# Kernel tuning notes

Hardware: AMD Instinct MI355X
Metric: run time of the kernel (lower is better)

Reference implementation:

```python
import jax, jax.numpy as jnp
import numpy as np

B, N, DIM = 16, 1024, 768


def setup_inputs() -> dict:
    key = jax.random.key(0)
    ks = jax.random.split(key, 8)
    x = jax.random.normal(ks[0], (B, N, DIM), dtype=jnp.float32)
    y = jax.random.normal(ks[1], (B, N, DIM), dtype=jnp.float32)
    coords = jax.random.normal(ks[2], (N, N, 6), dtype=jnp.float32)
    # orthogonal init for U (as in torch init.orthogonal_)
    a = jax.random.normal(ks[3], (DIM, DIM), dtype=jnp.float32)
    q, r = jnp.linalg.qr(a)
    U = q * jnp.sign(jnp.diagonal(r))[None, :]
    S1 = jnp.ones((DIM,), dtype=jnp.float32)
    S2 = jnp.ones((DIM,), dtype=jnp.float32)
    gating = jnp.asarray(1.0, dtype=jnp.float32)
    temp = jnp.asarray(0.1, dtype=jnp.float32)
    pos_emb = jnp.zeros((N, 6, 1), dtype=jnp.float32)
    return {"x": x, "y": y, "coords": coords, "U": U, "S1": S1, "S2": S2,
            "gating": gating, "temp": temp, "pos_emb": pos_emb}


def reference(x, y, coords, U, S1, S2, gating, temp, pos_emb):
    dim = x.shape[-1]
    scale = dim ** (-0.5)
    # spectral decomposition: x @ U^T @ diag(S^2) @ U
    xu = x @ U.T                                   # [B,N,d]
    x1 = (xu * jnp.square(S1)) @ U                 # [B,N,d]
    x2 = (xu * jnp.square(S2)) @ U                 # [B,N,d]
    xs = jnp.stack([x1, x2], axis=1)               # [B,2,N,d]
    patch_score = jax.nn.softmax(
        jnp.einsum('bknd,bmd->bknm', xs, y) * scale, axis=-1)  # [B,2,N,M]
    pos = jnp.squeeze(coords @ pos_emb, -1)        # [N,M]
    pos_score = jax.nn.softmax(pos, axis=-1)[None, None]        # [1,1,N,M]
    g = jax.nn.sigmoid(gating)
    attn = (1.0 - g) * patch_score + g * pos_score  # [B,2,N,M]
    # entropy-routed gating
    entropy = jnp.sum(-attn * jnp.log(attn + 1e-8), axis=-1)    # [B,2,N]
    hmap = 2.0 - 2.0 * jax.nn.sigmoid(temp * jnp.transpose(entropy, (0, 2, 1)))  # [B,N,2]
    fgbg = hmap[..., 0] >= hmap[..., 1]
    route = jax.lax.stop_gradient(
        jnp.stack([fgbg, ~fgbg], axis=-1).astype(hmap.dtype))   # [B,N,2]
    heat_map = jnp.sum(hmap * route, axis=-1, keepdims=True)    # [B,N,1]
    attn_c = jnp.sum(attn * jnp.transpose(route, (0, 2, 1))[..., None], axis=1)  # [B,N,M]
    out = attn_c @ y                               # [B,N,d]
    return (out, heat_map)
```

## Files before the change

### kernel.cpp

```cpp
#include <hip/hip_runtime.h>
#include <hip/hip_bf16.h>

#define DEV __device__ __forceinline__

typedef unsigned short u16;
typedef short short8 __attribute__((ext_vector_type(8)));
typedef float f32x16 __attribute__((ext_vector_type(16)));

static const int BB = 16;
static const int NN = 1024;
static const int DD = 768;

DEV u16 f2bf(float f) {
    unsigned u = __builtin_bit_cast(unsigned, f);
    unsigned r = u + 0x7fffu + ((u >> 16) & 1u);
    return (u16)(r >> 16);
}
DEV float h2f(u16 u) { return (float)__builtin_bit_cast(_Float16, u); }
DEV u16 f2h(float f) { return __builtin_bit_cast(u16, (_Float16)f); }

DEV short8 ldf8_bf(const float* p) {
    float4 f0 = *(const float4*)p;
    float4 f1 = *(const float4*)(p + 4);
    short8 r;
    r[0] = (short)f2bf(f0.x); r[1] = (short)f2bf(f0.y);
    r[2] = (short)f2bf(f0.z); r[3] = (short)f2bf(f0.w);
    r[4] = (short)f2bf(f1.x); r[5] = (short)f2bf(f1.y);
    r[6] = (short)f2bf(f1.z); r[7] = (short)f2bf(f1.w);
    return r;
}

DEV void gl_lds16(const void* g, void* l) {
    __builtin_amdgcn_global_load_lds(
        (const __attribute__((address_space(1))) unsigned int*)g,
        (__attribute__((address_space(3))) unsigned int*)l, 16, 0, 0);
}

DEV unsigned pkbf_rtz(float f0, float f1) {
    return __builtin_amdgcn_perm(__builtin_bit_cast(unsigned, f1),
                                 __builtin_bit_cast(unsigned, f0), 0x07060302u);
}

DEV void fence_bar() {
    asm volatile("" ::: "memory");
    __builtin_amdgcn_s_barrier();
    asm volatile("" ::: "memory");
}
DEV void wait_vm4() { asm volatile("s_waitcnt vmcnt(4)" ::: "memory"); }

template<int OM>
__global__ __launch_bounds__(256, 3) void gemm128(
    const u16* __restrict__ Ag, const u16* __restrict__ Bg, void* __restrict__ Cg,
    int K, int N, int zmod,
    long sA0, long sA1, long sB0, long sB1, long sC0, long sC1,
    float scale)
{
    __shared__ u16 As[128 * 64];
    __shared__ u16 Bs[128 * 64];

    int z = blockIdx.z;
    const u16* A = Ag + (long)(z % zmod) * sA0 + (long)(z / zmod) * sA1;
    const u16* B = Bg + (long)(z % zmod) * sB0 + (long)(z / zmod) * sB1;
    u16*   Cu = (u16*)Cg   + (long)(z % zmod) * sC0 + (long)(z / zmod) * sC1;
    float* Cf = (float*)Cg + (long)(z % zmod) * sC0 + (long)(z / zmod) * sC1;

    int tid  = threadIdx.x;
    int lane = tid & 63, wave = tid >> 6;
    int wm = wave & 1, wn = wave >> 1;
    int ln31 = lane & 31, khalf = lane >> 5;

    long m0 = (long)blockIdx.x * 128;
    long n0 = (long)blockIdx.y * 128;

    long aOfs[4], bOfs[4];
    u16 *lA[4], *lB[4];
#pragma unroll
    for (int i = 0; i < 4; i++) {
        int p = tid + i * 256;
        int row = p >> 3, qs = p & 7;
        int q = qs ^ (row & 7);
        aOfs[i] = (m0 + row) * (long)K + q * 8;
        bOfs[i] = (n0 + row) * (long)K + q * 8;
        lA[i] = As + p * 8;
        lB[i] = Bs + p * 8;
    }

    int aoff[2][4], boff[2][4];
#pragma unroll
    for (int t = 0; t < 2; t++) {
        int ra = wm * 64 + t * 32 + ln31;
        int rb = wn * 64 + t * 32 + ln31;
#pragma unroll
        for (int h = 0; h < 4; h++) {
            aoff[t][h] = ra * 64 + (((h * 2 + khalf) ^ (ra & 7)) * 8);
            boff[t][h] = rb * 64 + (((h * 2 + khalf) ^ (rb & 7)) * 8);
        }
    }

    f32x16 acc[2][2] = {};

    for (int k0 = 0; k0 < K; k0 += 64) {
#pragma unroll
        for (int i = 0; i < 4; i++) gl_lds16(A + aOfs[i] + k0, lA[i]);
#pragma unroll
        for (int i = 0; i < 4; i++) gl_lds16(B + bOfs[i] + k0, lB[i]);
        __syncthreads();

#pragma unroll
        for (int h = 0; h < 4; h++) {
            short8 af[2], bfr[2];
#pragma unroll
            for (int t = 0; t < 2; t++) af[t]  = *(const short8*)(As + aoff[t][h]);
#pragma unroll
            for (int t = 0; t < 2; t++) bfr[t] = *(const short8*)(Bs + boff[t][h]);
#pragma unroll
            for (int ti = 0; ti < 2; ti++)
#pragma unroll
                for (int tj = 0; tj < 2; tj++)
                    acc[ti][tj] = __builtin_amdgcn_mfma_f32_32x32x16_bf16(
                        af[ti], bfr[tj], acc[ti][tj], 0, 0, 0);
        }
        __syncthreads();
    }

    long crow = m0 + wm * 64 + 4 * khalf;
    long ccol = n0 + wn * 64 + ln31;
#pragma unroll
    for (int ti = 0; ti < 2; ti++)
#pragma unroll
        for (int tj = 0; tj < 2; tj++)
#pragma unroll
            for (int r = 0; r < 16; r++) {
                long row = crow + ti * 32 + (r & 3) + 8 * (r >> 2);
                long col = ccol + tj * 32;
                float v = acc[ti][tj][r] * scale;
                long idx = row * (long)N + col;
                if constexpr (OM == 0)      Cu[idx] = f2bf(v);
                else if constexpr (OM == 1) Cu[idx] = f2h(v);
                else                        Cf[idx] = v;
            }
}

template<int OM>
__global__ __launch_bounds__(512, 2) void gemm256(
    const u16* __restrict__ Ag, const u16* __restrict__ Bg, void* __restrict__ Cg,
    int K, int N, int zmod,
    long sA0, long sA1, long sB0, long sB1, long sC0, long sC1,
    float scale)
{
    __shared__ u16 lds[2][4][8192];

    int z = blockIdx.z;
    const u16* A = Ag + (long)(z % zmod) * sA0 + (long)(z / zmod) * sA1;
    const u16* B = Bg + (long)(z % zmod) * sB0 + (long)(z / zmod) * sB1;
    u16*   Cu = (u16*)Cg   + (long)(z % zmod) * sC0 + (long)(z / zmod) * sC1;
    float* Cf = (float*)Cg + (long)(z % zmod) * sC0 + (long)(z / zmod) * sC1;

    int tid  = threadIdx.x;
    int lane = tid & 63, wave = tid >> 6;
    int wm = wave >> 2, wn = wave & 3;
    int ln31 = lane & 31, khalf = lane >> 5;

    long m0 = (long)blockIdx.x * 256;
    long n0 = (long)blockIdx.y * 256;
    const u16* Apan = A + m0 * (long)K;
    const u16* Bpan = B + n0 * (long)K;

    long stA[2];
#pragma unroll
    for (int r = 0; r < 2; r++) {
        int p = tid + r * 512;
        int row = p >> 2, c = (p & 3) ^ ((row >> 1) & 3);
        stA[r] = (long)row * K + c * 8;
    }

    int aoffs[4][2], boffs[2][2];
#pragma unroll
    for (int m = 0; m < 4; m++) {
        int rr = wm * 128 + m * 32 + ln31;
#pragma unroll
        for (int sl = 0; sl < 2; sl++)
            aoffs[m][sl] = rr * 32 + (((sl * 2 + khalf) ^ ((rr >> 1) & 3)) * 8);
    }
#pragma unroll
    for (int n = 0; n < 2; n++) {
        int cc = wn * 64 + n * 32 + ln31;
#pragma unroll
        for (int sl = 0; sl < 2; sl++)
            boffs[n][sl] = cc * 32 + (((sl * 2 + khalf) ^ ((cc >> 1) & 3)) * 8);
    }

    f32x16 acc[4][2] = {};

    int nkt = K >> 6;
    int niter = nkt >> 1;

#define STG(PAN, BUF, HSEL, KT, KH) do {                                   \
    const u16* _s0 = (PAN) + stA[0] + (long)(KT) * 64 + (KH) * 32;         \
    const u16* _s1 = (PAN) + stA[1] + (long)(KT) * 64 + (KH) * 32;         \
    u16* _d = &lds[BUF][HSEL][0] + tid * 8;                                \
    gl_lds16(_s0, _d);                                                     \
    gl_lds16(_s1, _d + 4096);                                              \
} while (0)

#define PH(BUF, S, DOSTG, GUARD) do {                                      \
    short8 av[4], bv[2];                                                   \
    _Pragma("unroll")                                                      \
    for (int m = 0; m < 4; m++)                                            \
        av[m] = *(const short8*)(&lds[BUF][(S) >> 1][aoffs[m][(S) & 1]]);  \
    _Pragma("unroll")                                                      \
    for (int n = 0; n < 2; n++)                                            \
        bv[n] = *(const short8*)(&lds[BUF][2 + ((S) >> 1)][boffs[n][(S) & 1]]); \
    DOSTG;                                                                 \
    if (GUARD) wait_vm4();                                                 \
    fence_bar();                                                           \
    __builtin_amdgcn_s_setprio(1);                                         \
    _Pragma("unroll")                                                      \
    for (int m = 0; m < 4; m++)                                            \
        _Pragma("unroll")                                                  \
        for (int n = 0; n < 2; n++)                                        \
            acc[m][n] = __builtin_amdgcn_mfma_f32_32x32x16_bf16(           \
                av[m], bv[n], acc[m][n], 0, 0, 0);                         \
    __builtin_amdgcn_s_setprio(0);                                         \
    fence_bar();                                                           \
} while (0)

    STG(Apan, 0, 0, 0, 0);
    STG(Bpan, 0, 2, 0, 0);
    STG(Apan, 0, 1, 0, 1);
    STG(Bpan, 0, 3, 0, 1);
    STG(Apan, 1, 0, 1, 0);
    STG(Bpan, 1, 2, 1, 0);
    wait_vm4();
    fence_bar();

    for (int it = 0; it < niter; ++it) {
        int t1 = 2 * it + 1;
        int t2 = 2 * it + 2; int t2c = t2 < nkt ? t2 : nkt - 1;
        int t3 = 2 * it + 3; int t3c = t3 < nkt ? t3 : nkt - 1;
        PH(0, 0, STG(Apan, 1, 1, t1,  1), false);
        PH(0, 1, STG(Bpan, 1, 3, t1,  1), false);
        PH(0, 2, STG(Apan, 0, 0, t2c, 0), false);
        PH(0, 3, STG(Bpan, 0, 2, t2c, 0), true);
        PH(1, 0, STG(Apan, 0, 1, t2c, 1), false);
        PH(1, 1, STG(Bpan, 0, 3, t2c, 1), false);
        PH(1, 2, STG(Apan, 1, 0, t3c, 0), false);
        PH(1, 3, STG(Bpan, 1, 2, t3c, 0), true);
    }
#undef PH
#undef STG

    long crow = m0 + wm * 128 + 4 * khalf;
    long ccol = n0 + wn * 64 + ln31;
#pragma unroll
    for (int m = 0; m < 4; m++)
#pragma unroll
        for (int n = 0; n < 2; n++)
#pragma unroll
            for (int r = 0; r < 16; r++) {
                long row = crow + m * 32 + (r & 3) + 8 * (r >> 2);
                long col = ccol + n * 32;
                float v = acc[m][n][r] * scale;
                long idx = row * (long)N + col;
                if constexpr (OM == 0)      Cu[idx] = f2bf(v);
                else if constexpr (OM == 1) Cu[idx] = f2h(v);
                else                        Cf[idx] = v;
            }
}

__global__ __launch_bounds__(256, 3) void gemm_f32a(
    const float* __restrict__ Ag, const u16* __restrict__ Bg, u16* __restrict__ Cg,
    int K, int N, long sB0, long sC0)
{
    __shared__ float As[128 * 64];
    __shared__ u16   Bs[128 * 64];

    int z = blockIdx.z;
    const u16* B = Bg + (long)z * sB0;
    u16* Cu = Cg + (long)z * sC0;

    int tid  = threadIdx.x;
    int lane = tid & 63, wave = tid >> 6;
    int wm = wave & 1, wn = wave >> 1;
    int ln31 = lane & 31, khalf = lane >> 5;

    long m0 = (long)blockIdx.x * 128;
    long n0 = (long)blockIdx.y * 128;

    long aOfs[8]; float* lA[8];
#pragma unroll
    for (int i = 0; i < 8; i++) {
        int p = tid + i * 256;
        int row = p >> 4, q = (p & 15) ^ (row & 15);
        aOfs[i] = (m0 + row) * (long)K + q * 4;
        lA[i] = As + p * 4;
    }
    long bOfs[4]; u16* lB[4];
#pragma unroll
    for (int i = 0; i < 4; i++) {
        int p = tid + i * 256;
        int row = p >> 3, q = (p & 7) ^ (row & 7);
        bOfs[i] = (n0 + row) * (long)K + q * 8;
        lB[i] = Bs + p * 8;
    }

    int aoff[2][4][2], boff[2][4];
#pragma unroll
    for (int t = 0; t < 2; t++) {
        int ra = wm * 64 + t * 32 + ln31;
        int rb = wn * 64 + t * 32 + ln31;
#pragma unroll
        for (int h = 0; h < 4; h++) {
            int c0 = h * 4 + khalf * 2;
            aoff[t][h][0] = ra * 64 + ((c0 ^ (ra & 15)) * 4);
            aoff[t][h][1] = ra * 64 + (((c0 + 1) ^ (ra & 15)) * 4);
            boff[t][h] = rb * 64 + (((h * 2 + khalf) ^ (rb & 7)) * 8);
        }
    }

    f32x16 acc[2][2] = {};

    for (int k0 = 0; k0 < K; k0 += 64) {
#pragma unroll
        for (int i = 0; i < 8; i++) gl_lds16(Ag + aOfs[i] + k0, lA[i]);
#pragma unroll
        for (int i = 0; i < 4; i++) gl_lds16(B + bOfs[i] + k0, lB[i]);
        __syncthreads();

#pragma unroll
        for (int h = 0; h < 4; h++) {
            short8 af[2], bfr[2];
#pragma unroll
            for (int t = 0; t < 2; t++) {
                float4 v0 = *(const float4*)(As + aoff[t][h][0]);
                float4 v1 = *(const float4*)(As + aoff[t][h][1]);
                uint4 wv;
                wv.x = pkbf_rtz(v0.x, v0.y);
                wv.y = pkbf_rtz(v0.z, v0.w);
                wv.z = pkbf_rtz(v1.x, v1.y);
                wv.w = pkbf_rtz(v1.z, v1.w);
                af[t] = __builtin_bit_cast(short8, wv);
            }
#pragma unroll
            for (int t = 0; t < 2; t++) bfr[t] = *(const short8*)(Bs + boff[t][h]);
#pragma unroll
            for (int ti = 0; ti < 2; ti++)
#pragma unroll
                for (int tj = 0; tj < 2; tj++)
                    acc[ti][tj] = __builtin_amdgcn_mfma_f32_32x32x16_bf16(
                        af[ti], bfr[tj], acc[ti][tj], 0, 0, 0);
        }
        __syncthreads();
    }

    long crow = m0 + wm * 64 + 4 * khalf;
    long ccol = n0 + wn * 64 + ln31;
#pragma unroll
    for (int ti = 0; ti < 2; ti++)
#pragma unroll
        for (int tj = 0; tj < 2; tj++)
#pragma unroll
            for (int r = 0; r < 16; r++) {
                long row = crow + ti * 32 + (r & 3) + 8 * (r >> 2);
                long col = ccol + tj * 32;
                Cu[row * (long)N + col] = f2bf(acc[ti][tj][r]);
            }
}

DEV float wave_red_max(float v) {
#pragma unroll
    for (int o = 32; o; o >>= 1) v = fmaxf(v, __shfl_xor(v, o));
    return v;
}
DEV float wave_red_sum(float v) {
#pragma unroll
    for (int o = 32; o; o >>= 1) v += __shfl_xor(v, o);
    return v;
}
DEV float block_red_max(float v, float* sh) {
    v = wave_red_max(v);
    if ((threadIdx.x & 63) == 0) sh[threadIdx.x >> 6] = v;
    __syncthreads();
    v = fmaxf(fmaxf(sh[0], sh[1]), fmaxf(sh[2], sh[3]));
    __syncthreads();
    return v;
}
DEV float block_red_sum(float v, float* sh) {
    v = wave_red_sum(v);
    if ((threadIdx.x & 63) == 0) sh[threadIdx.x >> 6] = v;
    __syncthreads();
    v = (sh[0] + sh[1]) + (sh[2] + sh[3]);
    __syncthreads();
    return v;
}
DEV float red2_max(float v, float* sh) {
    v = wave_red_max(v);
    if ((threadIdx.x & 63) == 0) sh[threadIdx.x >> 6] = v;
    __syncthreads();
    v = fmaxf(sh[0], sh[1]);
    __syncthreads();
    return v;
}
DEV float red2_sum(float v, float* sh) {
    v = wave_red_sum(v);
    if ((threadIdx.x & 63) == 0) sh[threadIdx.x >> 6] = v;
    __syncthreads();
    v = sh[0] + sh[1];
    __syncthreads();
    return v;
}

__global__ __launch_bounds__(256) void k_prep_all(
    const float* __restrict__ y,
    const float* __restrict__ coords, const float* __restrict__ U,
    const float* __restrict__ S1, const float* __restrict__ S2,
    const float* __restrict__ pe,
    u16* __restrict__ yb, u16* __restrict__ yT,
    u16* __restrict__ UTb, u16* __restrict__ VT1, u16* __restrict__ VT2,
    float* __restrict__ P)
{
    __shared__ float shmem[32 * 33];
    int bid = blockIdx.x, tid = threadIdx.x;

    if (bid < 12288) {
        float (*tile)[33] = (float(*)[33])shmem;
        int b = bid / 768, rem = bid % 768;
        int d0 = (rem % 24) * 32, m0 = (rem / 24) * 32;
        int tx = tid & 31, ty = tid >> 5;
        const float* ybase = y + (long)b * NN * DD;
#pragma unroll
        for (int r = 0; r < 32; r += 8) {
            int m = m0 + ty + r, d = d0 + tx;
            float v = ybase[(long)m * DD + d];
            tile[ty + r][tx] = v;
            yb[(long)b * NN * DD + (long)m * DD + d] = f2bf(v);
        }
        __syncthreads();
#pragma unroll
        for (int r = 0; r < 32; r += 8) {
            int d = d0 + ty + r, m = m0 + tx;
            yT[(long)b * DD * NN + (long)d * NN + m] = f2bf(tile[tx][ty + r]);
        }
        return;
    }
    bid -= 12288;

    if (bid < 1024) {
        int n = bid, t = tid;
        float p6[6];
#pragma unroll
        for (int c = 0; c < 6; c++) p6[c] = pe[n * 6 + c];
        float v[4];
#pragma unroll
        for (int i = 0; i < 4; i++) {
            const float* cp = coords + ((long)n * NN + t * 4 + i) * 6;
            v[i] = p6[0]*cp[0] + p6[1]*cp[1] + p6[2]*cp[2]
                 + p6[3]*cp[3] + p6[4]*cp[4] + p6[5]*cp[5];
        }
        float mx = block_red_max(fmaxf(fmaxf(v[0], v[1]), fmaxf(v[2], v[3])), shmem);
        float e[4], s = 0.f;
#pragma unroll
        for (int i = 0; i < 4; i++) { e[i] = expf(v[i] - mx); s += e[i]; }
        float Z = block_red_sum(s, shmem);
        float inv = 1.f / Z;
        float4 o; o.x = e[0]*inv; o.y = e[1]*inv; o.z = e[2]*inv; o.w = e[3]*inv;
        *(float4*)(P + ((long)n << 10) + t * 4) = o;
        return;
    }
    bid -= 1024;

    {
        float (*tile)[33] = (float(*)[33])shmem;
        int i0 = (bid % 24) * 32, j0 = (bid / 24) * 32;
        int tx = tid & 31, ty = tid >> 5;
#pragma unroll
        for (int r = 0; r < 32; r += 8) {
            int i = i0 + ty + r, j = j0 + tx;
            tile[ty + r][tx] = U[(long)i * DD + j];
        }
        __syncthreads();
        float s1v = S1[i0 + tx];
        float s2v = S2[i0 + tx];
        s1v *= s1v; s2v *= s2v;
#pragma unroll
        for (int r = 0; r < 32; r += 8) {
            int j = j0 + ty + r, i = i0 + tx;
            float v = tile[tx][ty + r];
            UTb[(long)j * DD + i] = f2bf(v);
            VT1[(long)j * DD + i] = f2bf(s1v * v);
            VT2[(long)j * DD + i] = f2bf(s2v * v);
        }
    }
}

__global__ __launch_bounds__(128) void k_route(
    u16* __restrict__ S, const float* __restrict__ P,
    const float* __restrict__ gating, const float* __restrict__ temp,
    float* __restrict__ heat)
{
    __shared__ float sh[2];
    int bn = blockIdx.x;
    int b = bn >> 10, n = bn & 1023, t = threadIdx.x;
    u16* s1p = S + ((long)(b * 2) << 20) + ((long)n << 10) + t * 8;
    u16* s2p = s1p + (1L << 20);
    const float* pp = P + ((long)n << 10) + t * 8;

    short8 r1 = *(const short8*)s1p;
    short8 r2 = *(const short8*)s2p;
    float4 pv0 = *(const float4*)pp;
    float4 pv1 = *(const float4*)(pp + 4);
    float s1[8], s2[8], p8[8];
#pragma unroll
    for (int i = 0; i < 8; i++) {
        s1[i] = h2f((u16)r1[i]);
        s2[i] = h2f((u16)r2[i]);
    }
    p8[0]=pv0.x; p8[1]=pv0.y; p8[2]=pv0.z; p8[3]=pv0.w;
    p8[4]=pv1.x; p8[5]=pv1.y; p8[6]=pv1.z; p8[7]=pv1.w;

    float m1 = s1[0], m2 = s2[0];
#pragma unroll
    for (int i = 1; i < 8; i++) { m1 = fmaxf(m1, s1[i]); m2 = fmaxf(m2, s2[i]); }
    float mx1 = red2_max(m1, sh);
    float mx2 = red2_max(m2, sh);

    float e1[8], e2[8], z1 = 0.f, z2 = 0.f;
#pragma unroll
    for (int i = 0; i < 8; i++) {
        e1[i] = expf(s1[i] - mx1); z1 += e1[i];
        e2[i] = expf(s2[i] - mx2); z2 += e2[i];
    }
    float Z1 = red2_sum(z1, sh);
    float Z2 = red2_sum(z2, sh);

    float g = 1.f / (1.f + expf(-gating[0]));
    float c1 = (1.f - g) / Z1, c2 = (1.f - g) / Z2;

    float a1[8], a2[8], hh1 = 0.f, hh2 = 0.f;
#pragma unroll
    for (int i = 0; i < 8; i++) {
        a1[i] = e1[i] * c1 + g * p8[i];
        a2[i] = e2[i] * c2 + g * p8[i];
        hh1 -= a1[i] * logf(a1[i] + 1e-8f);
        hh2 -= a2[i] * logf(a2[i] + 1e-8f);
    }
    float H1 = red2_sum(hh1, sh);
    float H2 = red2_sum(hh2, sh);

    float tv = temp[0];
    float hm0 = 2.f - 2.f / (1.f + expf(-tv * H1));
    float hm1 = 2.f - 2.f / (1.f + expf(-tv * H2));
    int ks = (hm0 >= hm1) ? 0 : 1;
    if (t == 0) heat[bn] = ks ? hm1 : hm0;

    short8 w;
#pragma unroll
    for (int i = 0; i < 8; i++) w[i] = (short)f2bf(ks ? a2[i] : a1[i]);
    *(short8*)s1p = w;
}

extern "C" void kernel_launch(void* const* d_in, const int* in_sizes, int n_in,
                              void* d_out, int out_size, void* d_ws, size_t ws_size,
                              hipStream_t stream)
{
    (void)in_sizes; (void)n_in; (void)out_size; (void)ws_size;
    const float* x      = (const float*)d_in[0];
    const float* y      = (const float*)d_in[1];
    const float* coords = (const float*)d_in[2];
    const float* U      = (const float*)d_in[3];
    const float* S1     = (const float*)d_in[4];
    const float* S2     = (const float*)d_in[5];
    const float* gating = (const float*)d_in[6];
    const float* temp   = (const float*)d_in[7];
    const float* pose   = (const float*)d_in[8];

    float* out  = (float*)d_out;
    float* heat = out + (long)BB * NN * DD;

    char* w = (char*)d_ws;
    u16* UTb = (u16*)w;  w += (long)DD * DD * 2;
    u16* VT  = (u16*)w;  w += (long)2 * DD * DD * 2;
    u16* W2  = (u16*)w;  w += (long)2 * DD * DD * 2;
    u16* x12 = (u16*)w;  w += (long)2 * BB * NN * DD * 2;
    u16* yb  = (u16*)w;  w += (long)BB * NN * DD * 2;
    u16* yT  = (u16*)w;  w += (long)BB * DD * NN * 2;
    u16* S   = (u16*)w;  w += (long)BB * 2 * NN * NN * 2;
    float* P = (float*)w;

    const long MBN = (long)BB * NN * DD;
    const long BND = (long)NN * DD;
    const long SPL = (long)NN * NN;
    const long DSQ = (long)DD * DD;

    k_prep_all<<<dim3(13888), dim3(256), 0, stream>>>(
        y, coords, U, S1, S2, pose, yb, yT, UTb, VT, VT + DSQ, P);

    gemm128<0><<<dim3(DD / 128, DD / 128, 2), dim3(256), 0, stream>>>(
        UTb, VT, W2, DD, DD, 2,
        0L, 0L, DSQ, 0L, DSQ, 0L, 1.0f);

    gemm_f32a<<<dim3(BB * NN / 128, DD / 128, 2), dim3(256), 0, stream>>>(
        x, W2, x12, DD, DD, DSQ, MBN);

    gemm256<1><<<dim3(NN / 256, NN / 256, BB * 2), dim3(512), 0, stream>>>(
        x12, yb, S, DD, NN, 2,
        MBN, BND, 0L, BND, SPL, 2 * SPL, 0.036084391824351615f);

    k_route<<<dim3(BB * NN), dim3(128), 0, stream>>>(S, P, gating, temp, heat);

    gemm256<2><<<dim3(NN / 256, DD / 256, BB), dim3(512), 0, stream>>>(
        S, yT, out, NN, DD, 1,
        0L, 2 * SPL, 0L, BND, 0L, BND, 1.0f);
}
```

Before: 371.1 us.

## Pre-convert x to bf16 and use gemm256 for projection; single-wave routing

Adds an x-to-bf16 conversion stage inside the prep kernel, writing into the S workspace that is not yet in use. The x@W2 projection then runs through the larger bf16 gemm256 kernel in place of the fp32-A gemm128 variant that converted inside LDS. The y transpose/convert path is vectorised to float4 and u16x4 accesses. The routing kernel is shrunk to one 64-thread wave per row, with shuffle-only reductions in place of LDS-plus-barrier ones. The trade-off is an extra pass over x (fp32 read, bf16 write) and a change from truncating to round-to-nearest bf16 conversion of x.

```diff
diff --git a/kernel.cpp b/kernel.cpp
--- a/kernel.cpp
+++ b/kernel.cpp
@@ -5,6 +5,7 @@
 
 typedef unsigned short u16;
 typedef short short8 __attribute__((ext_vector_type(8)));
+typedef u16 u16x4 __attribute__((ext_vector_type(4)));
 typedef float f32x16 __attribute__((ext_vector_type(16)));
 
 static const int BB = 16;
@@ -19,26 +20,10 @@
 DEV float h2f(u16 u) { return (float)__builtin_bit_cast(_Float16, u); }
 DEV u16 f2h(float f) { return __builtin_bit_cast(u16, (_Float16)f); }
 
-DEV short8 ldf8_bf(const float* p) {
-    float4 f0 = *(const float4*)p;
-    float4 f1 = *(const float4*)(p + 4);
-    short8 r;
-    r[0] = (short)f2bf(f0.x); r[1] = (short)f2bf(f0.y);
-    r[2] = (short)f2bf(f0.z); r[3] = (short)f2bf(f0.w);
-    r[4] = (short)f2bf(f1.x); r[5] = (short)f2bf(f1.y);
-    r[6] = (short)f2bf(f1.z); r[7] = (short)f2bf(f1.w);
-    return r;
-}
-
 DEV void gl_lds16(const void* g, void* l) {
     __builtin_amdgcn_global_load_lds(
         (const __attribute__((address_space(1))) unsigned int*)g,
         (__attribute__((address_space(3))) unsigned int*)l, 16, 0, 0);
-}
-
-DEV unsigned pkbf_rtz(float f0, float f1) {
-    return __builtin_amdgcn_perm(__builtin_bit_cast(unsigned, f1),
-                                 __builtin_bit_cast(unsigned, f0), 0x07060302u);
 }
 
 DEV void fence_bar() {
@@ -268,105 +253,6 @@
             }
 }
 
-__global__ __launch_bounds__(256, 3) void gemm_f32a(
-    const float* __restrict__ Ag, const u16* __restrict__ Bg, u16* __restrict__ Cg,
-    int K, int N, long sB0, long sC0)
-{
-    __shared__ float As[128 * 64];
-    __shared__ u16   Bs[128 * 64];
-
-    int z = blockIdx.z;
-    const u16* B = Bg + (long)z * sB0;
-    u16* Cu = Cg + (long)z * sC0;
-
-    int tid  = threadIdx.x;
-    int lane = tid & 63, wave = tid >> 6;
-    int wm = wave & 1, wn = wave >> 1;
-    int ln31 = lane & 31, khalf = lane >> 5;
-
-    long m0 = (long)blockIdx.x * 128;
-    long n0 = (long)blockIdx.y * 128;
-
-    long aOfs[8]; float* lA[8];
-#pragma unroll
-    for (int i = 0; i < 8; i++) {
-        int p = tid + i * 256;
-        int row = p >> 4, q = (p & 15) ^ (row & 15);
-        aOfs[i] = (m0 + row) * (long)K + q * 4;
-        lA[i] = As + p * 4;
-    }
-    long bOfs[4]; u16* lB[4];
-#pragma unroll
-    for (int i = 0; i < 4; i++) {
-        int p = tid + i * 256;
-        int row = p >> 3, q = (p & 7) ^ (row & 7);
-        bOfs[i] = (n0 + row) * (long)K + q * 8;
-        lB[i] = Bs + p * 8;
-    }
-
-    int aoff[2][4][2], boff[2][4];
-#pragma unroll
-    for (int t = 0; t < 2; t++) {
-        int ra = wm * 64 + t * 32 + ln31;
-        int rb = wn * 64 + t * 32 + ln31;
-#pragma unroll
-        for (int h = 0; h < 4; h++) {
-            int c0 = h * 4 + khalf * 2;
-            aoff[t][h][0] = ra * 64 + ((c0 ^ (ra & 15)) * 4);
-            aoff[t][h][1] = ra * 64 + (((c0 + 1) ^ (ra & 15)) * 4);
-            boff[t][h] = rb * 64 + (((h * 2 + khalf) ^ (rb & 7)) * 8);
-        }
-    }
-
-    f32x16 acc[2][2] = {};
-
-    for (int k0 = 0; k0 < K; k0 += 64) {
-#pragma unroll
-        for (int i = 0; i < 8; i++) gl_lds16(Ag + aOfs[i] + k0, lA[i]);
-#pragma unroll
-        for (int i = 0; i < 4; i++) gl_lds16(B + bOfs[i] + k0, lB[i]);
-        __syncthreads();
-
-#pragma unroll
-        for (int h = 0; h < 4; h++) {
-            short8 af[2], bfr[2];
-#pragma unroll
-            for (int t = 0; t < 2; t++) {
-                float4 v0 = *(const float4*)(As + aoff[t][h][0]);
-                float4 v1 = *(const float4*)(As + aoff[t][h][1]);
-                uint4 wv;
-                wv.x = pkbf_rtz(v0.x, v0.y);
-                wv.y = pkbf_rtz(v0.z, v0.w);
-                wv.z = pkbf_rtz(v1.x, v1.y);
-                wv.w = pkbf_rtz(v1.z, v1.w);
-                af[t] = __builtin_bit_cast(short8, wv);
-            }
-#pragma unroll
-            for (int t = 0; t < 2; t++) bfr[t] = *(const short8*)(Bs + boff[t][h]);
-#pragma unroll
-            for (int ti = 0; ti < 2; ti++)
-#pragma unroll
-                for (int tj = 0; tj < 2; tj++)
-                    acc[ti][tj] = __builtin_amdgcn_mfma_f32_32x32x16_bf16(
-                        af[ti], bfr[tj], acc[ti][tj], 0, 0, 0);
-        }
-        __syncthreads();
-    }
-
-    long crow = m0 + wm * 64 + 4 * khalf;
-    long ccol = n0 + wn * 64 + ln31;
-#pragma unroll
-    for (int ti = 0; ti < 2; ti++)
-#pragma unroll
-        for (int tj = 0; tj < 2; tj++)
-#pragma unroll
-            for (int r = 0; r < 16; r++) {
-                long row = crow + ti * 32 + (r & 3) + 8 * (r >> 2);
-                long col = ccol + tj * 32;
-                Cu[row * (long)N + col] = f2bf(acc[ti][tj][r]);
-            }
-}
-
 DEV float wave_red_max(float v) {
 #pragma unroll
     for (int o = 32; o; o >>= 1) v = fmaxf(v, __shfl_xor(v, o));
@@ -393,29 +279,13 @@
     __syncthreads();
     return v;
 }
-DEV float red2_max(float v, float* sh) {
-    v = wave_red_max(v);
-    if ((threadIdx.x & 63) == 0) sh[threadIdx.x >> 6] = v;
-    __syncthreads();
-    v = fmaxf(sh[0], sh[1]);
-    __syncthreads();
-    return v;
-}
-DEV float red2_sum(float v, float* sh) {
-    v = wave_red_sum(v);
-    if ((threadIdx.x & 63) == 0) sh[threadIdx.x >> 6] = v;
-    __syncthreads();
-    v = sh[0] + sh[1];
-    __syncthreads();
-    return v;
-}
 
 __global__ __launch_bounds__(256) void k_prep_all(
-    const float* __restrict__ y,
+    const float* __restrict__ x, const float* __restrict__ y,
     const float* __restrict__ coords, const float* __restrict__ U,
     const float* __restrict__ S1, const float* __restrict__ S2,
     const float* __restrict__ pe,
-    u16* __restrict__ yb, u16* __restrict__ yT,
+    u16* __restrict__ xb, u16* __restrict__ yb, u16* __restrict__ yT,
     u16* __restrict__ UTb, u16* __restrict__ VT1, u16* __restrict__ VT2,
     float* __restrict__ P)
 {
@@ -426,24 +296,37 @@
         float (*tile)[33] = (float(*)[33])shmem;
         int b = bid / 768, rem = bid % 768;
         int d0 = (rem % 24) * 32, m0 = (rem / 24) * 32;
-        int tx = tid & 31, ty = tid >> 5;
+        int r = tid >> 3, c4 = (tid & 7) * 4;
         const float* ybase = y + (long)b * NN * DD;
-#pragma unroll
-        for (int r = 0; r < 32; r += 8) {
-            int m = m0 + ty + r, d = d0 + tx;
-            float v = ybase[(long)m * DD + d];
-            tile[ty + r][tx] = v;
-            yb[(long)b * NN * DD + (long)m * DD + d] = f2bf(v);
-        }
+        float4 v = *(const float4*)(ybase + (long)(m0 + r) * DD + d0 + c4);
+        u16x4 w4;
+        w4[0] = f2bf(v.x); w4[1] = f2bf(v.y); w4[2] = f2bf(v.z); w4[3] = f2bf(v.w);
+        *(u16x4*)(yb + (long)b * NN * DD + (long)(m0 + r) * DD + d0 + c4) = w4;
+        tile[r][c4 + 0] = v.x; tile[r][c4 + 1] = v.y;
+        tile[r][c4 + 2] = v.z; tile[r][c4 + 3] = v.w;
         __syncthreads();
-#pragma unroll
-        for (int r = 0; r < 32; r += 8) {
-            int d = d0 + ty + r, m = m0 + tx;
-            yT[(long)b * DD * NN + (long)d * NN + m] = f2bf(tile[tx][ty + r]);
-        }
+        int d = tid >> 3, mq = (tid & 7) * 4;
+        u16x4 o;
+        o[0] = f2bf(tile[mq + 0][d]); o[1] = f2bf(tile[mq + 1][d]);
+        o[2] = f2bf(tile[mq + 2][d]); o[3] = f2bf(tile[mq + 3][d]);
+        *(u16x4*)(yT + (long)b * DD * NN + (long)(d0 + d) * NN + m0 + mq) = o;
         return;
     }
     bid -= 12288;
+
+    if (bid < 6144) {
+        long base = ((long)bid * 256 + tid) * 8;
+        float4 f0 = *(const float4*)(x + base);
+        float4 f1 = *(const float4*)(x + base + 4);
+        short8 w;
+        w[0] = (short)f2bf(f0.x); w[1] = (short)f2bf(f0.y);
+        w[2] = (short)f2bf(f0.z); w[3] = (short)f2bf(f0.w);
+        w[4] = (short)f2bf(f1.x); w[5] = (short)f2bf(f1.y);
+        w[6] = (short)f2bf(f1.z); w[7] = (short)f2bf(f1.w);
+        *(short8*)(xb + base) = w;
+        return;
+    }
+    bid -= 6144;
 
     if (bid < 1024) {
         int n = bid, t = tid;
@@ -493,59 +376,67 @@
     }
 }
 
-__global__ __launch_bounds__(128) void k_route(
+__global__ __launch_bounds__(64) void k_route(
     u16* __restrict__ S, const float* __restrict__ P,
     const float* __restrict__ gating, const float* __restrict__ temp,
     float* __restrict__ heat)
 {
-    __shared__ float sh[2];
     int bn = blockIdx.x;
     int b = bn >> 10, n = bn & 1023, t = threadIdx.x;
-    u16* s1p = S + ((long)(b * 2) << 20) + ((long)n << 10) + t * 8;
+    u16* s1p = S + ((long)(b * 2) << 20) + ((long)n << 10);
     u16* s2p = s1p + (1L << 20);
-    const float* pp = P + ((long)n << 10) + t * 8;
-
-    short8 r1 = *(const short8*)s1p;
-    short8 r2 = *(const short8*)s2p;
-    float4 pv0 = *(const float4*)pp;
-    float4 pv1 = *(const float4*)(pp + 4);
-    float s1[8], s2[8], p8[8];
+    const float* pp = P + ((long)n << 10);
+
+    short8 r1a = *(const short8*)(s1p + t * 8);
+    short8 r1b = *(const short8*)(s1p + 512 + t * 8);
+    short8 r2a = *(const short8*)(s2p + t * 8);
+    short8 r2b = *(const short8*)(s2p + 512 + t * 8);
+    float4 pv0 = *(const float4*)(pp + t * 8);
+    float4 pv1 = *(const float4*)(pp + t * 8 + 4);
+    float4 pv2 = *(const float4*)(pp + 512 + t * 8);
+    float4 pv3 = *(const float4*)(pp + 512 + t * 8 + 4);
+
+    float s1[16], s2[16], p8[16];
 #pragma unroll
     for (int i = 0; i < 8; i++) {
-        s1[i] = h2f((u16)r1[i]);
-        s2[i] = h2f((u16)r2[i]);
-    }
-    p8[0]=pv0.x; p8[1]=pv0.y; p8[2]=pv0.z; p8[3]=pv0.w;
-    p8[4]=pv1.x; p8[5]=pv1.y; p8[6]=pv1.z; p8[7]=pv1.w;
+        s1[i]     = h2f((u16)r1a[i]);
+        s1[i + 8] = h2f((u16)r1b[i]);
+        s2[i]     = h2f((u16)r2a[i]);
+        s2[i + 8] = h2f((u16)r2b[i]);
+    }
+    p8[0]=pv0.x;  p8[1]=pv0.y;  p8[2]=pv0.z;  p8[3]=pv0.w;
+    p8[4]=pv1.x;  p8[5]=pv1.y;  p8[6]=pv1.z;  p8[7]=pv1.w;
+    p8[8]=pv2.x;  p8[9]=pv2.y;  p8[10]=pv2.z; p8[11]=pv2.w;
+    p8[12]=pv3.x; p8[13]=pv3.y; p8[14]=pv3.z; p8[15]=pv3.w;
 
     float m1 = s1[0], m2 = s2[0];
 #pragma unroll
-    for (int i = 1; i < 8; i++) { m1 = fmaxf(m1, s1[i]); m2 = fmaxf(m2, s2[i]); }
-    float mx1 = red2_max(m1, sh);
-    float mx2 = red2_max(m2, sh);
-
-    float e1[8], e2[8], z1 = 0.f, z2 = 0.f;
-#pragma unroll
-    for (int i = 0; i < 8; i++) {
+    for (int i = 1; i < 16; i++) { m1 = fmaxf(m1, s1[i]); m2 = fmaxf(m2, s2[i]); }
+    float mx1 = wave_red_max(m1);
+    float mx2 = wave_red_max(m2);
+
+    float e1[16], e2[16], z1 = 0.f, z2 = 0.f;
+#pragma unroll
+    for (int i = 0; i < 16; i++) {
         e1[i] = expf(s1[i] - mx1); z1 += e1[i];
         e2[i] = expf(s2[i] - mx2); z2 += e2[i];
     }
-    float Z1 = red2_sum(z1, sh);
-    float Z2 = red2_sum(z2, sh);
+    float Z1 = wave_red_sum(z1);
+    float Z2 = wave_red_sum(z2);
 
     float g = 1.f / (1.f + expf(-gating[0]));
     float c1 = (1.f - g) / Z1, c2 = (1.f - g) / Z2;
 
-    float a1[8], a2[8], hh1 = 0.f, hh2 = 0.f;
-#pragma unroll
-    for (int i = 0; i < 8; i++) {
+    float a1[16], a2[16], hh1 = 0.f, hh2 = 0.f;
+#pragma unroll
+    for (int i = 0; i < 16; i++) {
         a1[i] = e1[i] * c1 + g * p8[i];
         a2[i] = e2[i] * c2 + g * p8[i];
         hh1 -= a1[i] * logf(a1[i] + 1e-8f);
         hh2 -= a2[i] * logf(a2[i] + 1e-8f);
     }
-    float H1 = red2_sum(hh1, sh);
-    float H2 = red2_sum(hh2, sh);
+    float H1 = wave_red_sum(hh1);
+    float H2 = wave_red_sum(hh2);
 
     float tv = temp[0];
     float hm0 = 2.f - 2.f / (1.f + expf(-tv * H1));
@@ -553,10 +444,14 @@
     int ks = (hm0 >= hm1) ? 0 : 1;
     if (t == 0) heat[bn] = ks ? hm1 : hm0;
 
-    short8 w;
-#pragma unroll
-    for (int i = 0; i < 8; i++) w[i] = (short)f2bf(ks ? a2[i] : a1[i]);
-    *(short8*)s1p = w;
+    short8 w0, w1;
+#pragma unroll
+    for (int i = 0; i < 8; i++) {
+        w0[i] = (short)f2bf(ks ? a2[i] : a1[i]);
+        w1[i] = (short)f2bf(ks ? a2[i + 8] : a1[i + 8]);
+    }
+    *(short8*)(s1p + t * 8) = w0;
+    *(short8*)(s1p + 512 + t * 8) = w1;
 }
 
 extern "C" void kernel_launch(void* const* d_in, const int* in_sizes, int n_in,
@@ -587,26 +482,29 @@
     u16* S   = (u16*)w;  w += (long)BB * 2 * NN * NN * 2;
     float* P = (float*)w;
 
+    u16* xb = S;
+
     const long MBN = (long)BB * NN * DD;
     const long BND = (long)NN * DD;
     const long SPL = (long)NN * NN;
     const long DSQ = (long)DD * DD;
 
-    k_prep_all<<<dim3(13888), dim3(256), 0, stream>>>(
-        y, coords, U, S1, S2, pose, yb, yT, UTb, VT, VT + DSQ, P);
+    k_prep_all<<<dim3(20032), dim3(256), 0, stream>>>(
+        x, y, coords, U, S1, S2, pose, xb, yb, yT, UTb, VT, VT + DSQ, P);
 
     gemm128<0><<<dim3(DD / 128, DD / 128, 2), dim3(256), 0, stream>>>(
         UTb, VT, W2, DD, DD, 2,
         0L, 0L, DSQ, 0L, DSQ, 0L, 1.0f);
 
-    gemm_f32a<<<dim3(BB * NN / 128, DD / 128, 2), dim3(256), 0, stream>>>(
-        x, W2, x12, DD, DD, DSQ, MBN);
+    gemm256<0><<<dim3(BB * NN / 256, DD / 256, 2), dim3(512), 0, stream>>>(
+        xb, W2, x12, DD, DD, 2,
+        0L, 0L, DSQ, 0L, MBN, 0L, 1.0f);
 
     gemm256<1><<<dim3(NN / 256, NN / 256, BB * 2), dim3(512), 0, stream>>>(
         x12, yb, S, DD, NN, 2,
         MBN, BND, 0L, BND, SPL, 2 * SPL, 0.036084391824351615f);
 
-    k_route<<<dim3(BB * NN), dim3(128), 0, stream>>>(S, P, gating, temp, heat);
+    k_route<<<dim3(BB * NN), dim3(64), 0, stream>>>(S, P, gating, temp, heat);
 
     gemm256<2><<<dim3(NN / 256, DD / 256, BB), dim3(512), 0, stream>>>(
         S, yT, out, NN, DD, 1,
```

Result: faster. 362.5 us (-2.3%).
